# Kernel tuning notes

Measured on AMD Instinct MI355X. Metric: run time of the kernel, lower is better.

Reference implementation:

```python
import jax, jax.numpy as jnp
import numpy as np

D = 12      # depth
C = 768     # embed_dim
NH = 12     # num_heads
P = 16      # patch_size
IMG = 224
G = IMG // P          # 14 patch grid
N = G * G + 1         # 197 tokens (CLS + patches)
WIN = 7               # window_size
NC = 1000             # num_classes
HID = 3072            # mlp hidden


def _local_mask():
    m = np.zeros((N, N), dtype=bool)
    m[0, :] = True
    m[:, 0] = True
    idx = np.arange(N - 1)
    r = idx // G
    c = idx % G
    half = WIN // 2
    m[1:, 1:] = (np.abs(r[:, None] - r[None, :]) <= half) & (np.abs(c[:, None] - c[None, :]) <= half)
    return jnp.asarray(m)

MASK = _local_mask()


def _ln(x, w, b, eps=1e-5):
    mu = x.mean(-1, keepdims=True)
    var = ((x - mu) ** 2).mean(-1, keepdims=True)
    return (x - mu) / jnp.sqrt(var + eps) * w + b


def setup_inputs() -> dict:
    key = jax.random.key(0)
    ks = jax.random.split(key, 16)
    s = jnp.float32(0.02)
    B = 32
    return {
        "x": jax.random.normal(ks[0], (B, 3, IMG, IMG), jnp.float32),
        "patch_w": jax.random.normal(ks[1], (C, 3, P, P), jnp.float32) * s,
        "patch_b": jnp.zeros((C,), jnp.float32),
        "cls_token": jax.random.normal(ks[2], (1, 1, C), jnp.float32) * s,
        "pos_embed": jax.random.normal(ks[3], (1, N, C), jnp.float32) * s,
        "ln1_w": jnp.ones((D, C), jnp.float32),
        "ln1_b": jnp.zeros((D, C), jnp.float32),
        "qkv_w": jax.random.normal(ks[4], (D, C, 3 * C), jnp.float32) * s,
        "proj_w": jax.random.normal(ks[5], (D, C, C), jnp.float32) * s,
        "proj_b": jnp.zeros((D, C), jnp.float32),
        "ln2_w": jnp.ones((D, C), jnp.float32),
        "ln2_b": jnp.zeros((D, C), jnp.float32),
        "mlp_w1": jax.random.normal(ks[6], (D, C, HID), jnp.float32) * s,
        "mlp_b1": jnp.zeros((D, HID), jnp.float32),
        "mlp_w2": jax.random.normal(ks[7], (D, HID, C), jnp.float32) * s,
        "mlp_b2": jnp.zeros((D, C), jnp.float32),
        "norm_w": jnp.ones((C,), jnp.float32),
        "norm_b": jnp.zeros((C,), jnp.float32),
        "head_w": jax.random.normal(ks[8], (C, NC), jnp.float32) * s,
        "head_b": jnp.zeros((NC,), jnp.float32),
    }


def reference(x, patch_w, patch_b, cls_token, pos_embed, ln1_w, ln1_b, qkv_w,
              proj_w, proj_b, ln2_w, ln2_b, mlp_w1, mlp_b1, mlp_w2, mlp_b2,
              norm_w, norm_b, head_w, head_b):
    B = x.shape[0]
    hd = C // NH
    scale = hd ** -0.5
    # Patch embed (Conv2d stride=kernel == non-overlapping patch matmul)
    xp = x.reshape(B, 3, G, P, G, P).transpose(0, 2, 4, 1, 3, 5).reshape(B, G * G, 3 * P * P)
    t = xp @ patch_w.reshape(C, 3 * P * P).T + patch_b
    t = jnp.concatenate([jnp.broadcast_to(cls_token, (B, 1, C)), t], axis=1) + pos_embed
    for i in range(D):
        h = _ln(t, ln1_w[i], ln1_b[i])
        qkv = (h @ qkv_w[i]).reshape(B, N, 3, NH, hd)
        q, k, v = qkv[:, :, 0], qkv[:, :, 1], qkv[:, :, 2]  # (B,N,NH,hd)
        attn = jnp.einsum('bqhd,bkhd->bhqk', q, k) * scale
        attn = jnp.where(MASK, attn, -jnp.inf)
        attn = jax.nn.softmax(attn, axis=-1)
        o = jnp.einsum('bhqk,bkhd->bqhd', attn, v).reshape(B, N, C)
        t = t + o @ proj_w[i] + proj_b[i]
        h = _ln(t, ln2_w[i], ln2_b[i])
        h = jax.nn.gelu(h @ mlp_w1[i] + mlp_b1[i], approximate=False)
        t = t + h @ mlp_w2[i] + mlp_b2[i]
    t = _ln(t, norm_w, norm_b)
    return t[:, 0] @ head_w + head_b
```

## Files before the change

### kernel.cpp

```cpp
#include <hip/hip_runtime.h>
#include <hip/hip_bf16.h>
#include <math.h>

#define Dn 12
#define Cc 768
#define NHh 12
#define HD 64
#define Gg 14
#define Nn_TOK 197
#define HID 3072
#define NC 1000
#define Bb 32

typedef __attribute__((ext_vector_type(8))) short short8;
typedef __attribute__((ext_vector_type(4))) float f32x4;

__device__ __forceinline__ ushort f2b(float v) {
    union { float f; unsigned u; } x; x.f = v;
    unsigned r = x.u + 0x7fff + ((x.u >> 16) & 1);
    return (ushort)(r >> 16);
}
__device__ __forceinline__ float b2f(ushort v) {
    union { unsigned u; float f; } x; x.u = ((unsigned)v) << 16; return x.f;
}
__device__ __forceinline__ void gld16(const void* g, void* s) {
    __builtin_amdgcn_global_load_lds(
        (const __attribute__((address_space(1))) void*)g,
        (__attribute__((address_space(3))) void*)s, 16, 0, 0);
}

__global__ void im2col_kernel(const float* __restrict__ x, ushort* __restrict__ xp) {
    size_t idx = (size_t)blockIdx.x * 256 + threadIdx.x;
    const size_t total = (size_t)Bb * 196 * 768;
    if (idx >= total) return;
    int j = idx % 768;
    size_t t0 = idx / 768;
    int g = t0 % 196;
    int b = t0 / 196;
    int ch = j / 256, rem = j % 256, pr = rem / 16, pc = rem % 16;
    int gr = g / Gg, gc = g % Gg;
    int row = gr * 16 + pr, col = gc * 16 + pc;
    xp[idx] = f2b(x[(((size_t)b * 3 + ch) * 224 + row) * 224 + col]);
}

__global__ void assemble_kernel(const float* __restrict__ pe, const float* __restrict__ cls,
                                const float* __restrict__ pos, float* __restrict__ t) {
    size_t idx = (size_t)blockIdx.x * 256 + threadIdx.x;
    const size_t total = (size_t)Bb * Nn_TOK * 768;
    if (idx >= total) return;
    int c = idx % 768;
    size_t r = idx / 768;
    int n = r % Nn_TOK, b = r / Nn_TOK;
    float v;
    if (n == 0) v = cls[c];
    else       v = pe[((size_t)b * 196 + (n - 1)) * 768 + c];
    t[idx] = v + pos[(size_t)n * 768 + c];
}

__global__ void cvt_kernel(const float* __restrict__ src, ushort* __restrict__ dst, int n) {
    int idx = blockIdx.x * 256 + threadIdx.x;
    if (idx < n) dst[idx] = f2b(src[idx]);
}

__global__ __launch_bounds__(256) void transpose_one(const float* __restrict__ src,
                                                     ushort* __restrict__ dst, int K, int N) {
    int k0 = blockIdx.x * 32, n0 = blockIdx.y * 32;
    __shared__ float tile[32][33];
    int tx = threadIdx.x & 31, ty = threadIdx.x >> 5;
    #pragma unroll
    for (int r = ty; r < 32; r += 8)
        if (k0 + r < K && n0 + tx < N)
            tile[r][tx] = src[(size_t)(k0 + r) * N + n0 + tx];
    __syncthreads();
    #pragma unroll
    for (int r = ty; r < 32; r += 8)
        if (n0 + r < N && k0 + tx < K)
            dst[(size_t)(n0 + r) * K + k0 + tx] = f2b(tile[tx][r]);
}

__global__ __launch_bounds__(256) void transpose4_kernel(
    const float* __restrict__ qkvw, const float* __restrict__ projw,
    const float* __restrict__ w1, const float* __restrict__ w2,
    ushort* __restrict__ dq, ushort* __restrict__ dp,
    ushort* __restrict__ d1, ushort* __restrict__ d2)
{
    int tile = blockIdx.x;
    const float* src; ushort* dst; int N, kt, nt;
    if (tile < 1728)      { src = qkvw; dst = dq; N = 2304; kt = tile / 72; nt = tile % 72; }
    else if (tile < 2304) { tile -= 1728; src = projw; dst = dp; N = 768; kt = tile / 24; nt = tile % 24; }
    else if (tile < 4608) { tile -= 2304; src = w1; dst = d1; N = 3072; kt = tile / 96; nt = tile % 96; }
    else                  { tile -= 4608; src = w2; dst = d2; N = 768; kt = tile / 24; nt = tile % 24; }
    int K = (dst == d2) ? 3072 : 768;
    int k0 = kt * 32, n0 = nt * 32;
    __shared__ float tilebuf[32][33];
    int tx = threadIdx.x & 31, ty = threadIdx.x >> 5;
    #pragma unroll
    for (int r = ty; r < 32; r += 8)
        tilebuf[r][tx] = src[(size_t)(k0 + r) * N + n0 + tx];
    __syncthreads();
    #pragma unroll
    for (int r = ty; r < 32; r += 8)
        dst[(size_t)(n0 + r) * K + k0 + tx] = f2b(tilebuf[tx][r]);
}

#define TM 128
#define TN 128
__global__ __launch_bounds__(256) void gemm_bf16(
    const ushort* __restrict__ A, const ushort* __restrict__ B,
    void* __restrict__ outp, const float* __restrict__ bias,
    const float* __restrict__ residual, int M, int N, int K, int flags)
{
    __shared__ ushort As[4][128][8];
    __shared__ ushort Bs[4][128][8];
    const int tid = threadIdx.x;
    const int wave = tid >> 6, lane = tid & 63;
    const int br = blockIdx.y * TM, bc = blockIdx.x * TN;
    const int wm = (wave >> 1) * 64, wn = (wave & 1) * 64;

    const int hA0 = tid >> 7, rA0 = tid & 127;
    const int hA1 = (tid + 256) >> 7;
    const ushort* pA0 = A + (size_t)min(br + rA0, M - 1) * K + hA0 * 8;
    const ushort* pA1 = A + (size_t)min(br + rA0, M - 1) * K + hA1 * 8;
    const ushort* pB0 = B + (size_t)min(bc + rA0, N - 1) * K + hA0 * 8;
    const ushort* pB1 = B + (size_t)min(bc + rA0, N - 1) * K + hA1 * 8;
    ushort* sA0 = &As[0][0][0] + (size_t)(wave * 64) * 8;
    ushort* sA1 = &As[0][0][0] + (size_t)(256 + wave * 64) * 8;
    ushort* sB0 = &Bs[0][0][0] + (size_t)(wave * 64) * 8;
    ushort* sB1 = &Bs[0][0][0] + (size_t)(256 + wave * 64) * 8;

    f32x4 acc[4][4];
    #pragma unroll
    for (int i = 0; i < 4; ++i)
        #pragma unroll
        for (int j = 0; j < 4; ++j) acc[i][j] = (f32x4){0.f, 0.f, 0.f, 0.f};

    const int h = lane >> 4, m16 = lane & 15;
    const int nk = K >> 5;
    for (int kt = 0; kt < nk; ++kt) {
        __syncthreads();
        gld16(pA0, sA0); gld16(pA1, sA1);
        gld16(pB0, sB0); gld16(pB1, sB1);
        pA0 += 32; pA1 += 32; pB0 += 32; pB1 += 32;
        __syncthreads();
        short8 af[4], bfr[4];
        #pragma unroll
        for (int i = 0; i < 4; ++i) af[i]  = *(const short8*)&As[h][wm + i * 16 + m16][0];
        #pragma unroll
        for (int j = 0; j < 4; ++j) bfr[j] = *(const short8*)&Bs[h][wn + j * 16 + m16][0];
        #pragma unroll
        for (int i = 0; i < 4; ++i)
            #pragma unroll
            for (int j = 0; j < 4; ++j)
                acc[i][j] = __builtin_amdgcn_mfma_f32_16x16x32_bf16(af[i], bfr[j], acc[i][j], 0, 0, 0);
    }

    const bool obf = (flags & 2) != 0, gelu = (flags & 1) != 0;
    const int q = lane >> 4, cx = lane & 15;
    #pragma unroll
    for (int j = 0; j < 4; ++j) {
        int gc = bc + wn + j * 16 + cx;
        if (gc >= N) continue;
        float bv = bias ? bias[gc] : 0.f;
        #pragma unroll
        for (int i = 0; i < 4; ++i) {
            #pragma unroll
            for (int r = 0; r < 4; ++r) {
                int gr = br + wm + i * 16 + q * 4 + r;
                if (gr >= M) continue;
                float v = acc[i][j][r] + bv;
                if (gelu) v = 0.5f * v * (1.f + erff(v * 0.70710678118654752f));
                size_t off = (size_t)gr * N + gc;
                if (residual) v += residual[off];
                if (obf) ((ushort*)outp)[off] = f2b(v);
                else     ((float*)outp)[off] = v;
            }
        }
    }
}

__global__ __launch_bounds__(256) void ln_kernel(
    const float* __restrict__ in, ushort* __restrict__ out,
    const float* __restrict__ w, const float* __restrict__ b, long in_stride)
{
    int row = blockIdx.x;
    const float* xr = in + (size_t)row * in_stride;
    ushort* orow = out + (size_t)row * 768;
    int tid = threadIdx.x;
    float vals[3];
    float s = 0.f, s2 = 0.f;
    #pragma unroll
    for (int l = 0; l < 3; ++l) {
        float v = xr[tid + l * 256];
        vals[l] = v; s += v; s2 += v * v;
    }
    __shared__ float sh[256];
    __shared__ float stats[2];
    sh[tid] = s; __syncthreads();
    for (int o = 128; o > 0; o >>= 1) { if (tid < o) sh[tid] += sh[tid + o]; __syncthreads(); }
    if (tid == 0) stats[0] = sh[0];
    __syncthreads();
    sh[tid] = s2; __syncthreads();
    for (int o = 128; o > 0; o >>= 1) { if (tid < o) sh[tid] += sh[tid + o]; __syncthreads(); }
    if (tid == 0) stats[1] = sh[0];
    __syncthreads();
    float mean = stats[0] * (1.f / 768.f);
    float var = stats[1] * (1.f / 768.f) - mean * mean;
    float rstd = rsqrtf(var + 1e-5f);
    #pragma unroll
    for (int l = 0; l < 3; ++l) {
        int c = tid + l * 256;
        orow[c] = f2b((vals[l] - mean) * rstd * w[c] + b[c]);
    }
}

#define VST 232
__global__ __launch_bounds__(256) void attn_kernel(
    const ushort* __restrict__ qkv, ushort* __restrict__ out)
{
    const int h = blockIdx.x, b = blockIdx.y, zs = blockIdx.z;
    __shared__ ushort Vsh[64][VST];
    __shared__ ushort Psh[4][16][VST];
    const int tid = threadIdx.x, wave = tid >> 6, lane = tid & 63;
    const size_t base = (size_t)b * Nn_TOK * 2304 + (size_t)h * 64;

    {
        short8* vf = (short8*)&Vsh[0][0];
        for (int i = tid; i < 64 * VST / 8; i += 256)
            vf[i] = (short8){0, 0, 0, 0, 0, 0, 0, 0};
    }
    __syncthreads();
    for (int idx = tid; idx < Nn_TOK * 32; idx += 256) {
        int n = idx >> 5, d2 = (idx & 31) * 2;
        unsigned u = *(const unsigned*)(qkv + base + 1536 + (size_t)n * 2304 + d2);
        Vsh[d2][n]     = (ushort)(u & 0xffffu);
        Vsh[d2 + 1][n] = (ushort)(u >> 16);
    }
    *(unsigned long long*)&Psh[wave][lane >> 2][208 + (lane & 3) * 4] = 0ull;
    __syncthreads();

    const int kcol = lane & 15, lhi = lane >> 4;
    int rk[14], ck[14]; bool kin[14], kwin[14];
    #pragma unroll
    for (int kt = 0; kt < 14; ++kt) {
        int k = kt * 16 + kcol;
        kin[kt]  = (k < Nn_TOK);
        kwin[kt] = (k >= 1) && (k < Nn_TOK);
        int km1 = k - 1;
        rk[kt] = km1 / 14;
        ck[kt] = km1 - rk[kt] * 14;
    }
    const bool kcls = (kcol == 0);

    const int tlo = zs ? 7 : 0, thi = zs ? 13 : 7;
    for (int qt = tlo + wave; qt < thi; qt += 4) {
        const int qbase = qt * 16;
        const int qrow = qbase + kcol;
        const ushort* qp = qkv + base + (size_t)min(qrow, Nn_TOK - 1) * 2304 + lhi * 8;
        const short8 qf0 = *(const short8*)qp;
        const short8 qf1 = *(const short8*)(qp + 32);

        f32x4 S[14];
        #pragma unroll
        for (int kt = 0; kt < 14; ++kt) {
            int krow = min(kt * 16 + kcol, Nn_TOK - 1);
            const ushort* kp = qkv + base + 768 + (size_t)krow * 2304 + lhi * 8;
            short8 kf0 = *(const short8*)kp;
            short8 kf1 = *(const short8*)(kp + 32);
            f32x4 s = (f32x4){0.f, 0.f, 0.f, 0.f};
            s = __builtin_amdgcn_mfma_f32_16x16x32_bf16(qf0, kf0, s, 0, 0, 0);
            s = __builtin_amdgcn_mfma_f32_16x16x32_bf16(qf1, kf1, s, 0, 0, 0);
            S[kt] = s;
        }

        int rq_[4], cq_[4]; bool qc_[4];
        #pragma unroll
        for (int r = 0; r < 4; ++r) {
            int q = qbase + lhi * 4 + r;
            qc_[r] = (q == 0);
            int qm1 = q - 1;
            rq_[r] = qm1 / 14;
            cq_[r] = qm1 - rq_[r] * 14;
        }
        #pragma unroll
        for (int kt = 0; kt < 14; ++kt)
            #pragma unroll
            for (int r = 0; r < 4; ++r) {
                unsigned dr = (unsigned)(rq_[r] - rk[kt] + 3);
                unsigned dc = (unsigned)(cq_[r] - ck[kt] + 3);
                bool ok = (kwin[kt] && dr <= 6u && dc <= 6u)
                          || (qc_[r] && kin[kt]) || (kt == 0 && kcls);
                S[kt][r] = ok ? S[kt][r] : -1e30f;
            }

        float mx[4] = {-1e30f, -1e30f, -1e30f, -1e30f};
        #pragma unroll
        for (int kt = 0; kt < 14; ++kt)
            #pragma unroll
            for (int r = 0; r < 4; ++r) mx[r] = fmaxf(mx[r], S[kt][r]);
        #pragma unroll
        for (int r = 0; r < 4; ++r) {
            #pragma unroll
            for (int o = 8; o > 0; o >>= 1) mx[r] = fmaxf(mx[r], __shfl_xor(mx[r], o));
        }
        float ls[4] = {0.f, 0.f, 0.f, 0.f};
        #pragma unroll
        for (int kt = 0; kt < 14; ++kt)
            #pragma unroll
            for (int r = 0; r < 4; ++r) {
                float p = __expf((S[kt][r] - mx[r]) * 0.125f);
                S[kt][r] = p; ls[r] += p;
            }
        #pragma unroll
        for (int r = 0; r < 4; ++r) {
            #pragma unroll
            for (int o = 8; o > 0; o >>= 1) ls[r] += __shfl_xor(ls[r], o);
            ls[r] = 1.f / ls[r];
        }

        #pragma unroll
        for (int kt = 0; kt < 13; ++kt)
            #pragma unroll
            for (int r = 0; r < 4; ++r)
                Psh[wave][lhi * 4 + r][kt * 16 + kcol] = f2b(S[kt][r] * ls[r]);

        f32x4 O[4];
        #pragma unroll
        for (int j = 0; j < 4; ++j) O[j] = (f32x4){0.f, 0.f, 0.f, 0.f};
        #pragma unroll
        for (int ks = 0; ks < 7; ++ks) {
            short8 pf = *(const short8*)&Psh[wave][kcol][ks * 32 + lhi * 8];
            #pragma unroll
            for (int j = 0; j < 4; ++j) {
                short8 vfr = *(const short8*)&Vsh[j * 16 + kcol][ks * 32 + lhi * 8];
                O[j] = __builtin_amdgcn_mfma_f32_16x16x32_bf16(pf, vfr, O[j], 0, 0, 0);
            }
        }

        #pragma unroll
        for (int r = 0; r < 4; ++r) {
            int q = qbase + lhi * 4 + r;
            if (q < Nn_TOK) {
                size_t orow = ((size_t)b * Nn_TOK + q) * 768 + (size_t)h * 64;
                #pragma unroll
                for (int j = 0; j < 4; ++j)
                    out[orow + j * 16 + kcol] = f2b(O[j][r]);
            }
        }
    }
}

extern "C" void kernel_launch(void* const* d_in, const int* in_sizes, int n_in,
                              void* d_out, int out_size, void* d_ws, size_t ws_size,
                              hipStream_t stream) {
    const float* x        = (const float*)d_in[0];
    const float* patch_w  = (const float*)d_in[1];
    const float* patch_b  = (const float*)d_in[2];
    const float* cls_tok  = (const float*)d_in[3];
    const float* pos_emb  = (const float*)d_in[4];
    const float* ln1_w    = (const float*)d_in[5];
    const float* ln1_b    = (const float*)d_in[6];
    const float* qkv_w    = (const float*)d_in[7];
    const float* proj_w   = (const float*)d_in[8];
    const float* proj_b   = (const float*)d_in[9];
    const float* ln2_w    = (const float*)d_in[10];
    const float* ln2_b    = (const float*)d_in[11];
    const float* mlp_w1   = (const float*)d_in[12];
    const float* mlp_b1   = (const float*)d_in[13];
    const float* mlp_w2   = (const float*)d_in[14];
    const float* mlp_b2   = (const float*)d_in[15];
    const float* norm_w   = (const float*)d_in[16];
    const float* norm_b   = (const float*)d_in[17];
    const float* head_w   = (const float*)d_in[18];
    const float* head_b   = (const float*)d_in[19];
    float* out = (float*)d_out;

    char* ws = (char*)d_ws;
    float*  t     = (float*)ws;
    float*  pbuf  = (float*)(ws + 19365888);
    ushort* abuf  = (ushort*)(ws + 38633472);
    ushort* qbuf  = (ushort*)(ws + 48316416);
    ushort* hbuf  = (ushort*)(ws + 77365248);
    ushort* wq    = (ushort*)(ws + 116097024);
    ushort* wp    = wq + 1769472;
    ushort* w1t   = wp + 589824;
    ushort* w2t   = w1t + 2359296;
    ushort* pwbuf = (ushort*)(ws + 130252800);
    ushort* hwbuf = (ushort*)(ws + 131432448);

    const int M_tok = Bb * Nn_TOK;

    {
        size_t total = (size_t)Bb * 196 * 768;
        im2col_kernel<<<dim3((total + 255) / 256), 256, 0, stream>>>(x, abuf);
    }
    cvt_kernel<<<dim3((589824 + 255) / 256), 256, 0, stream>>>(patch_w, pwbuf, 589824);
    transpose_one<<<dim3(24, 32), 256, 0, stream>>>(head_w, hwbuf, 768, NC);
    gemm_bf16<<<dim3(6, 49), 256, 0, stream>>>(abuf, pwbuf, pbuf, patch_b, nullptr, Bb * 196, Cc, Cc, 0);
    {
        size_t total = (size_t)M_tok * 768;
        assemble_kernel<<<dim3((total + 255) / 256), 256, 0, stream>>>(pbuf, cls_tok, pos_emb, t);
    }

    for (int i = 0; i < Dn; ++i) {
        transpose4_kernel<<<dim3(6912), 256, 0, stream>>>(
            qkv_w + (size_t)i * Cc * 3 * Cc, proj_w + (size_t)i * Cc * Cc,
            mlp_w1 + (size_t)i * Cc * HID, mlp_w2 + (size_t)i * HID * Cc,
            wq, wp, w1t, w2t);
        ln_kernel<<<dim3(M_tok), 256, 0, stream>>>(t, abuf, ln1_w + i * Cc, ln1_b + i * Cc, Cc);
        gemm_bf16<<<dim3(18, 50), 256, 0, stream>>>(abuf, wq, qbuf, nullptr, nullptr, M_tok, 3 * Cc, Cc, 2);
        attn_kernel<<<dim3(NHh, Bb, 2), 256, 0, stream>>>(qbuf, abuf);
        gemm_bf16<<<dim3(6, 50), 256, 0, stream>>>(abuf, wp, t, proj_b + i * Cc, t, M_tok, Cc, Cc, 0);
        ln_kernel<<<dim3(M_tok), 256, 0, stream>>>(t, abuf, ln2_w + i * Cc, ln2_b + i * Cc, Cc);
        gemm_bf16<<<dim3(24, 50), 256, 0, stream>>>(abuf, w1t, hbuf, mlp_b1 + i * HID, nullptr, M_tok, HID, Cc, 3);
        gemm_bf16<<<dim3(6, 50), 256, 0, stream>>>(hbuf, w2t, t, mlp_b2 + i * Cc, t, M_tok, Cc, HID, 0);
    }

    ln_kernel<<<dim3(Bb), 256, 0, stream>>>(t, abuf, norm_w, norm_b, (long)Nn_TOK * Cc);
    gemm_bf16<<<dim3(8, 1), 256, 0, stream>>>(abuf, hwbuf, out, head_b, nullptr, Bb, NC, Cc, 0);
}
```

Before: 5.725 ms.

## Double-buffer GEMM LDS tiles and swizzle workgroups across XCDs

The bf16 GEMM now keeps two LDS buffers and issues the global-to-LDS loads for the next K tile before computing on the current one, using explicit vmcnt waits and raw barriers so memory latency can overlap the MFMA work. It also remaps the linear block index so that consecutive tiles land on the same XCD, aiming at better L2 reuse of shared A/B rows. The cost is twice the LDS per block, which may lower occupancy, and hand-written waitcnt logic that depends on how many loads gld16 issues.

```diff
diff --git a/kernel.cpp b/kernel.cpp
--- a/kernel.cpp
+++ b/kernel.cpp
@@ -110,11 +110,19 @@
     void* __restrict__ outp, const float* __restrict__ bias,
     const float* __restrict__ residual, int M, int N, int K, int flags)
 {
-    __shared__ ushort As[4][128][8];
-    __shared__ ushort Bs[4][128][8];
+    __shared__ ushort As[2][4][128][8];
+    __shared__ ushort Bs[2][4][128][8];
     const int tid = threadIdx.x;
     const int wave = tid >> 6, lane = tid & 63;
-    const int br = blockIdx.y * TM, bc = blockIdx.x * TN;
+
+    const int nwg = gridDim.x * gridDim.y;
+    const int orig = blockIdx.y * gridDim.x + blockIdx.x;
+    const int xcd = orig & 7, loc = orig >> 3;
+    const int q8 = nwg >> 3, r8 = nwg & 7;
+    const int swz = (xcd < r8 ? xcd * (q8 + 1) : r8 * (q8 + 1) + (xcd - r8) * q8) + loc;
+    const int bx = swz % gridDim.x, by = swz / gridDim.x;
+
+    const int br = by * TM, bc = bx * TN;
     const int wm = (wave >> 1) * 64, wn = (wave & 1) * 64;
 
     const int hA0 = tid >> 7, rA0 = tid & 127;
@@ -123,10 +131,11 @@
     const ushort* pA1 = A + (size_t)min(br + rA0, M - 1) * K + hA1 * 8;
     const ushort* pB0 = B + (size_t)min(bc + rA0, N - 1) * K + hA0 * 8;
     const ushort* pB1 = B + (size_t)min(bc + rA0, N - 1) * K + hA1 * 8;
-    ushort* sA0 = &As[0][0][0] + (size_t)(wave * 64) * 8;
-    ushort* sA1 = &As[0][0][0] + (size_t)(256 + wave * 64) * 8;
-    ushort* sB0 = &Bs[0][0][0] + (size_t)(wave * 64) * 8;
-    ushort* sB1 = &Bs[0][0][0] + (size_t)(256 + wave * 64) * 8;
+    ushort* sA0 = &As[0][0][0][0] + (size_t)(wave * 64) * 8;
+    ushort* sA1 = &As[0][0][0][0] + (size_t)(256 + wave * 64) * 8;
+    ushort* sB0 = &Bs[0][0][0][0] + (size_t)(wave * 64) * 8;
+    ushort* sB1 = &Bs[0][0][0][0] + (size_t)(256 + wave * 64) * 8;
+    const size_t BUFO = 4096;
 
     f32x4 acc[4][4];
     #pragma unroll
@@ -136,22 +145,37 @@
 
     const int h = lane >> 4, m16 = lane & 15;
     const int nk = K >> 5;
+
+    gld16(pA0, sA0); gld16(pA1, sA1);
+    gld16(pB0, sB0); gld16(pB1, sB1);
+
     for (int kt = 0; kt < nk; ++kt) {
-        __syncthreads();
-        gld16(pA0, sA0); gld16(pA1, sA1);
-        gld16(pB0, sB0); gld16(pB1, sB1);
-        pA0 += 32; pA1 += 32; pB0 += 32; pB1 += 32;
-        __syncthreads();
+        const int cur = kt & 1;
+        if (kt + 1 < nk) {
+            const size_t ko = (size_t)(kt + 1) * 32;
+            const size_t bo = (size_t)((kt + 1) & 1) * BUFO;
+            gld16(pA0 + ko, sA0 + bo); gld16(pA1 + ko, sA1 + bo);
+            gld16(pB0 + ko, sB0 + bo); gld16(pB1 + ko, sB1 + bo);
+            asm volatile("s_waitcnt vmcnt(4)" ::: "memory");
+        } else {
+            asm volatile("s_waitcnt vmcnt(0)" ::: "memory");
+        }
+        __builtin_amdgcn_s_barrier();
+
         short8 af[4], bfr[4];
         #pragma unroll
-        for (int i = 0; i < 4; ++i) af[i]  = *(const short8*)&As[h][wm + i * 16 + m16][0];
-        #pragma unroll
-        for (int j = 0; j < 4; ++j) bfr[j] = *(const short8*)&Bs[h][wn + j * 16 + m16][0];
+        for (int i = 0; i < 4; ++i) af[i]  = *(const short8*)&As[cur][h][wm + i * 16 + m16][0];
+        #pragma unroll
+        for (int j = 0; j < 4; ++j) bfr[j] = *(const short8*)&Bs[cur][h][wn + j * 16 + m16][0];
         #pragma unroll
         for (int i = 0; i < 4; ++i)
             #pragma unroll
             for (int j = 0; j < 4; ++j)
                 acc[i][j] = __builtin_amdgcn_mfma_f32_16x16x32_bf16(af[i], bfr[j], acc[i][j], 0, 0, 0);
+
+        asm volatile("s_waitcnt lgkmcnt(0)" ::: "memory");
+        __builtin_amdgcn_sched_barrier(0);
+        __builtin_amdgcn_s_barrier();
     }
 
     const bool obf = (flags & 2) != 0, gelu = (flags & 1) != 0;
```

New measurement: 5.474 ms. 1.05x faster.
